# Optimization experiments

Measured on AMD Instinct MI355X. Metric: run time of the kernel, lower is better.

The kernel has to match this reference:

```python
import jax, jax.numpy as jnp
import numpy as np

B, N, D = 4, 128, 128
EPS = 1e-6

def setup_inputs() -> dict:
    key = jax.random.key(0)
    ks = jax.random.split(key, 10)
    q = jax.random.normal(ks[0], (B, N, D), dtype=jnp.float32)
    mu = jax.random.normal(ks[1], (B, N, 3, D), dtype=jnp.float32)
    Wij = jax.random.normal(ks[2], (B, N, N, 3 * D), dtype=jnp.float32)
    dir_ij = jax.random.normal(ks[3], (B, N, N, 3), dtype=jnp.float32)
    mask_ij = jax.random.uniform(ks[4], (B, N, N), dtype=jnp.float32)
    # RMSNorm weight initialized to zeros (torch code: nn.Parameter(torch.zeros(dim)))
    norm_w = jnp.zeros((D,), dtype=jnp.float32)
    # Dense 1 (GLU variant): Linear(D, 2D)
    s1 = 1.0 / np.sqrt(D)
    W1 = jax.random.uniform(ks[5], (2 * D, D), minval=-s1, maxval=s1, dtype=jnp.float32)
    b1 = jax.random.uniform(ks[6], (2 * D,), minval=-s1, maxval=s1, dtype=jnp.float32)
    # Dense 2: Linear(D, 3D), no activation
    W2 = jax.random.uniform(ks[7], (3 * D, D), minval=-s1, maxval=s1, dtype=jnp.float32)
    b2 = jax.random.uniform(ks[8], (3 * D,), minval=-s1, maxval=s1, dtype=jnp.float32)
    return {"q": q, "mu": mu, "Wij": Wij, "dir_ij": dir_ij, "mask_ij": mask_ij,
            "norm_w": norm_w, "W1": W1, "b1": b1, "W2": W2, "b2": b2}

def reference(q, mu, Wij, dir_ij, mask_ij, norm_w, W1, b1, W2, b2):
    # RMSNorm (fp32, unit offset)
    xf = q.astype(jnp.float32)
    var = jnp.mean(xf * xf, axis=-1, keepdims=True)
    h = xf * jax.lax.rsqrt(var + EPS) * (1.0 + norm_w)
    # Dense(D -> D, GLU with silu) then Dense(D -> 3D)
    y = h @ W1.T + b1                      # (B,N,2D)
    a, g = jnp.split(y, 2, axis=-1)
    h2 = jax.nn.silu(a) * jax.nn.sigmoid(g)
    x = h2 @ W2.T + b2                     # (B,N,3D)
    # pairwise broadcast-multiply: xj over neighbor axis j
    x_inter = Wij * x[:, None, :, :] * mask_ij[..., None]   # (B,N,N,3D)
    dq, dmuR, dmumu = jnp.split(x_inter, 3, axis=-1)        # each (B,N,N,D)
    dq = dq.sum(axis=2)                                     # (B,N,D)
    muj = jnp.swapaxes(mu, -1, -2)[:, None]                 # (B,1,N,D,3)
    dmu = (dmuR[..., None] * dir_ij[:, :, :, None, :]
           + dmumu[..., None] * muj).sum(axis=2)            # (B,N,D,3)
    dmu = jnp.swapaxes(dmu, -1, -2)                         # (B,N,3,D)
    return (q + dq, mu + dmu)
```

## Files before the change

kernel.cpp:

```cpp
#include <hip/hip_runtime.h>


#define B_ 4
#define N_ 128
#define D_ 128

typedef __attribute__((ext_vector_type(4))) float float4v;

__device__ __align__(16) float g_x[B_ * N_ * 3 * D_];

__device__ __forceinline__ float sigm(float x) { return 1.0f / (1.0f + __expf(-x)); }

__global__ __launch_bounds__(256) void k1_mlp(
        const float* __restrict__ q, const float* __restrict__ norm_w,
        const float* __restrict__ W1, const float* __restrict__ b1,
        const float* __restrict__ W2, const float* __restrict__ b2) {
    const int row = blockIdx.x;
    const int t   = threadIdx.x;

    __shared__ __align__(16) float hbuf[D_];
    __shared__ __align__(16) float h2buf[D_];
    __shared__ float ybuf[2 * D_];
    __shared__ float red4[4];

    float v  = (t < D_) ? q[(size_t)row * D_ + t] : 0.0f;
    float ss = v * v;
    #pragma unroll
    for (int off = 32; off > 0; off >>= 1) ss += __shfl_down(ss, off);
    if ((t & 63) == 0) red4[t >> 6] = ss;
    __syncthreads();
    float var   = (red4[0] + red4[1] + red4[2] + red4[3]) * (1.0f / D_);
    float scale = rsqrtf(var + 1e-6f);
    if (t < D_) hbuf[t] = v * scale * (1.0f + norm_w[t]);
    __syncthreads();

    float y = b1[t];
    const float4v* wr = (const float4v*)(W1 + (size_t)t * D_);
    #pragma unroll 8
    for (int c = 0; c < D_ / 4; ++c) {
        float4v w4 = wr[c];
        float4v h4 = *(const float4v*)&hbuf[4 * c];
        y += w4.x * h4.x + w4.y * h4.y + w4.z * h4.z + w4.w * h4.w;
    }
    ybuf[t] = y;
    __syncthreads();
    if (t < D_) {
        float a = ybuf[t], g = ybuf[D_ + t];
        h2buf[t] = a * sigm(a) * sigm(g);
    }
    __syncthreads();

    float x0 = b2[t];
    float x1 = (t < D_) ? b2[2 * D_ + t] : 0.0f;
    const float4v* w0 = (const float4v*)(W2 + (size_t)t * D_);
    const float4v* w1 = (const float4v*)(W2 + (size_t)(2 * D_ + (t & (D_ - 1))) * D_);
    #pragma unroll 8
    for (int c = 0; c < D_ / 4; ++c) {
        float4v h4 = *(const float4v*)&h2buf[4 * c];
        float4v a4 = w0[c];
        x0 += a4.x * h4.x + a4.y * h4.y + a4.z * h4.z + a4.w * h4.w;
        if (t < D_) {
            float4v b4 = w1[c];
            x1 += b4.x * h4.x + b4.y * h4.y + b4.z * h4.z + b4.w * h4.w;
        }
    }
    float* xr = g_x + (size_t)row * (3 * D_);
    xr[t] = x0;
    if (t < D_) xr[2 * D_ + t] = x1;
}

__global__ __launch_bounds__(512) void k2_pair(
        const float* __restrict__ q, const float* __restrict__ mu,
        const float* __restrict__ Wij, const float* __restrict__ dir,
        const float* __restrict__ mask, float* __restrict__ out) {
    const int blk  = blockIdx.x;
    const int t    = threadIdx.x;
    const int quad = t & 31;
    const int js   = t >> 5;
    const int b    = blk >> 7;

    const float* Wb  = Wij  + (size_t)blk * (N_ * 3 * D_);
    const float* mb  = mask + (size_t)blk * N_;
    const float* db  = dir  + (size_t)blk * (N_ * 3);
    const float* mub = mu   + (size_t)b * (N_ * 3 * D_);
    const float* xb  = g_x  + (size_t)b * (N_ * 3 * D_);

    float4v aq = {0.f, 0.f, 0.f, 0.f};
    float4v a0 = {0.f, 0.f, 0.f, 0.f};
    float4v a1 = {0.f, 0.f, 0.f, 0.f};
    float4v a2 = {0.f, 0.f, 0.f, 0.f};

    #pragma unroll 2
    for (int it = 0; it < 8; ++it) {
        const int j = it * 16 + js;
        const float m  = mb[j];
        const float e0 = db[3 * j + 0];
        const float e1 = db[3 * j + 1];
        const float e2 = db[3 * j + 2];

        const size_t base = (size_t)j * (3 * D_) + 4 * quad;
        float4v wq = __builtin_nontemporal_load((const float4v*)(Wb + base));
        float4v wR = __builtin_nontemporal_load((const float4v*)(Wb + base + D_));
        float4v wm = __builtin_nontemporal_load((const float4v*)(Wb + base + 2 * D_));
        float4v xq = *(const float4v*)(xb + base);
        float4v xR = *(const float4v*)(xb + base + D_);
        float4v xm = *(const float4v*)(xb + base + 2 * D_);
        float4v u0 = *(const float4v*)(mub + base);
        float4v u1 = *(const float4v*)(mub + base + D_);
        float4v u2 = *(const float4v*)(mub + base + 2 * D_);

        #pragma unroll
        for (int i = 0; i < 4; ++i) {
            aq[i] += wq[i] * (xq[i] * m);
            float tR = wR[i] * (xR[i] * m);
            float tm = wm[i] * (xm[i] * m);
            a0[i] += tR * e0 + tm * u0[i];
            a1[i] += tR * e1 + tm * u1[i];
            a2[i] += tR * e2 + tm * u2[i];
        }
    }

    #pragma unroll
    for (int i = 0; i < 4; ++i) {
        aq[i] += __shfl_down(aq[i], 32);
        a0[i] += __shfl_down(a0[i], 32);
        a1[i] += __shfl_down(a1[i], 32);
        a2[i] += __shfl_down(a2[i], 32);
    }

    __shared__ __align__(16) float ws[8][4][D_];
    const int w = t >> 6, l = t & 63;
    if (l < 32) {
        *(float4v*)&ws[w][0][4 * quad] = aq;
        *(float4v*)&ws[w][1][4 * quad] = a0;
        *(float4v*)&ws[w][2][4 * quad] = a1;
        *(float4v*)&ws[w][3][4 * quad] = a2;
    }
    __syncthreads();

    const int comp = t >> 7;
    const int ch   = t & 127;
    float s = 0.f;
    #pragma unroll
    for (int wv = 0; wv < 8; ++wv) s += ws[wv][comp][ch];

    if (comp == 0) {
        const size_t o = (size_t)blk * D_ + ch;
        __builtin_nontemporal_store(q[o] + s, out + o);
    } else {
        const size_t o = ((size_t)blk * 3 + (comp - 1)) * D_ + ch;
        __builtin_nontemporal_store(mu[o] + s, out + (size_t)(B_ * N_ * D_) + o);
    }
}

extern "C" void kernel_launch(void* const* d_in, const int* in_sizes, int n_in,
                              void* d_out, int out_size, void* d_ws, size_t ws_size,
                              hipStream_t stream) {
    const float* q     = (const float*)d_in[0];
    const float* mu    = (const float*)d_in[1];
    const float* Wij   = (const float*)d_in[2];
    const float* dir   = (const float*)d_in[3];
    const float* mask  = (const float*)d_in[4];
    const float* normw = (const float*)d_in[5];
    const float* W1    = (const float*)d_in[6];
    const float* b1    = (const float*)d_in[7];
    const float* W2    = (const float*)d_in[8];
    const float* b2    = (const float*)d_in[9];

    k1_mlp <<<B_ * N_, 256, 0, stream>>>(q, normw, W1, b1, W2, b2);
    k2_pair<<<B_ * N_, 512, 0, stream>>>(q, mu, Wij, dir, mask, (float*)d_out);
}
```

Before: 195.7 us.

## Split pair kernel across channel halves with register prefetch and staged mask/dir

The pair kernel now launches twice as many 256-thread blocks, each covering half the channels of one (b,i) row. It stages mask and direction values into shared memory and software-pipelines the Wij/x/mu loads one iteration ahead in registers. The reduction switches to xor shuffles plus a smaller shared buffer. The aim is more blocks in flight and more memory-level parallelism for the dominant Wij stream, at the cost of higher register pressure and duplicated x/mu reads across the two halves.

```diff
diff --git a/kernel.cpp b/kernel.cpp
--- a/kernel.cpp
+++ b/kernel.cpp
@@ -69,86 +69,122 @@
     if (t < D_) xr[2 * D_ + t] = x1;
 }
 
-__global__ __launch_bounds__(512) void k2_pair(
+__global__ __launch_bounds__(256, 4) void k2_pair(
         const float* __restrict__ q, const float* __restrict__ mu,
         const float* __restrict__ Wij, const float* __restrict__ dir,
         const float* __restrict__ mask, float* __restrict__ out) {
     const int blk  = blockIdx.x;
+    const int bi   = blk >> 1;
+    const int h    = blk & 1;
+    const int b    = bi >> 7;
     const int t    = threadIdx.x;
-    const int quad = t & 31;
-    const int js   = t >> 5;
-    const int b    = blk >> 7;
-
-    const float* Wb  = Wij  + (size_t)blk * (N_ * 3 * D_);
-    const float* mb  = mask + (size_t)blk * N_;
-    const float* db  = dir  + (size_t)blk * (N_ * 3);
+    const int quad = t & 15;
+    const int js   = t >> 4;
+    const int choff = h * 64 + 4 * quad;
+
+    const float* Wb  = Wij  + (size_t)bi * (N_ * 3 * D_);
     const float* mub = mu   + (size_t)b * (N_ * 3 * D_);
     const float* xb  = g_x  + (size_t)b * (N_ * 3 * D_);
+
+    __shared__ float smsk[N_];
+    __shared__ float sdir[3 * N_];
+    {
+        const float* mb = mask + (size_t)bi * N_;
+        const float* db = dir  + (size_t)bi * (N_ * 3);
+        if (t < N_) smsk[t] = mb[t];
+        for (int idx = t; idx < 3 * N_; idx += 256) sdir[idx] = db[idx];
+    }
+    __syncthreads();
 
     float4v aq = {0.f, 0.f, 0.f, 0.f};
     float4v a0 = {0.f, 0.f, 0.f, 0.f};
     float4v a1 = {0.f, 0.f, 0.f, 0.f};
     float4v a2 = {0.f, 0.f, 0.f, 0.f};
 
-    #pragma unroll 2
+    float4v wqA, wRA, wmA, xqA, xRA, xmA, u0A, u1A, u2A;
+    float4v wqB, wRB, wmB, xqB, xRB, xmB, u0B, u1B, u2B;
+
+    {
+        const size_t base = (size_t)js * (3 * D_) + choff;
+        wqA = __builtin_nontemporal_load((const float4v*)(Wb + base));
+        wRA = __builtin_nontemporal_load((const float4v*)(Wb + base + D_));
+        wmA = __builtin_nontemporal_load((const float4v*)(Wb + base + 2 * D_));
+        xqA = *(const float4v*)(xb + base);
+        xRA = *(const float4v*)(xb + base + D_);
+        xmA = *(const float4v*)(xb + base + 2 * D_);
+        u0A = *(const float4v*)(mub + base);
+        u1A = *(const float4v*)(mub + base + D_);
+        u2A = *(const float4v*)(mub + base + 2 * D_);
+    }
+
+    #pragma unroll
     for (int it = 0; it < 8; ++it) {
+        if (it < 7) {
+            const int jn = (it + 1) * 16 + js;
+            const size_t base = (size_t)jn * (3 * D_) + choff;
+            wqB = __builtin_nontemporal_load((const float4v*)(Wb + base));
+            wRB = __builtin_nontemporal_load((const float4v*)(Wb + base + D_));
+            wmB = __builtin_nontemporal_load((const float4v*)(Wb + base + 2 * D_));
+            xqB = *(const float4v*)(xb + base);
+            xRB = *(const float4v*)(xb + base + D_);
+            xmB = *(const float4v*)(xb + base + 2 * D_);
+            u0B = *(const float4v*)(mub + base);
+            u1B = *(const float4v*)(mub + base + D_);
+            u2B = *(const float4v*)(mub + base + 2 * D_);
+        }
+
         const int j = it * 16 + js;
-        const float m  = mb[j];
-        const float e0 = db[3 * j + 0];
-        const float e1 = db[3 * j + 1];
-        const float e2 = db[3 * j + 2];
-
-        const size_t base = (size_t)j * (3 * D_) + 4 * quad;
-        float4v wq = __builtin_nontemporal_load((const float4v*)(Wb + base));
-        float4v wR = __builtin_nontemporal_load((const float4v*)(Wb + base + D_));
-        float4v wm = __builtin_nontemporal_load((const float4v*)(Wb + base + 2 * D_));
-        float4v xq = *(const float4v*)(xb + base);
-        float4v xR = *(const float4v*)(xb + base + D_);
-        float4v xm = *(const float4v*)(xb + base + 2 * D_);
-        float4v u0 = *(const float4v*)(mub + base);
-        float4v u1 = *(const float4v*)(mub + base + D_);
-        float4v u2 = *(const float4v*)(mub + base + 2 * D_);
+        const float m  = smsk[j];
+        const float e0 = sdir[3 * j + 0];
+        const float e1 = sdir[3 * j + 1];
+        const float e2 = sdir[3 * j + 2];
 
         #pragma unroll
         for (int i = 0; i < 4; ++i) {
-            aq[i] += wq[i] * (xq[i] * m);
-            float tR = wR[i] * (xR[i] * m);
-            float tm = wm[i] * (xm[i] * m);
-            a0[i] += tR * e0 + tm * u0[i];
-            a1[i] += tR * e1 + tm * u1[i];
-            a2[i] += tR * e2 + tm * u2[i];
+            aq[i] += wqA[i] * (xqA[i] * m);
+            float tR = wRA[i] * (xRA[i] * m);
+            float tm = wmA[i] * (xmA[i] * m);
+            a0[i] += tR * e0 + tm * u0A[i];
+            a1[i] += tR * e1 + tm * u1A[i];
+            a2[i] += tR * e2 + tm * u2A[i];
         }
+
+        wqA = wqB; wRA = wRB; wmA = wmB;
+        xqA = xqB; xRA = xRB; xmA = xmB;
+        u0A = u0B; u1A = u1B; u2A = u2B;
     }
 
     #pragma unroll
     for (int i = 0; i < 4; ++i) {
-        aq[i] += __shfl_down(aq[i], 32);
-        a0[i] += __shfl_down(a0[i], 32);
-        a1[i] += __shfl_down(a1[i], 32);
-        a2[i] += __shfl_down(a2[i], 32);
-    }
-
-    __shared__ __align__(16) float ws[8][4][D_];
+        aq[i] += __shfl_xor(aq[i], 16, 64);
+        aq[i] += __shfl_xor(aq[i], 32, 64);
+        a0[i] += __shfl_xor(a0[i], 16, 64);
+        a0[i] += __shfl_xor(a0[i], 32, 64);
+        a1[i] += __shfl_xor(a1[i], 16, 64);
+        a1[i] += __shfl_xor(a1[i], 32, 64);
+        a2[i] += __shfl_xor(a2[i], 16, 64);
+        a2[i] += __shfl_xor(a2[i], 32, 64);
+    }
+
+    __shared__ __align__(16) float ws[4][4][64];
     const int w = t >> 6, l = t & 63;
-    if (l < 32) {
-        *(float4v*)&ws[w][0][4 * quad] = aq;
-        *(float4v*)&ws[w][1][4 * quad] = a0;
-        *(float4v*)&ws[w][2][4 * quad] = a1;
-        *(float4v*)&ws[w][3][4 * quad] = a2;
-    }
-    __syncthreads();
-
-    const int comp = t >> 7;
-    const int ch   = t & 127;
-    float s = 0.f;
-    #pragma unroll
-    for (int wv = 0; wv < 8; ++wv) s += ws[wv][comp][ch];
+    if (l < 16) {
+        *(float4v*)&ws[w][0][4 * l] = aq;
+        *(float4v*)&ws[w][1][4 * l] = a0;
+        *(float4v*)&ws[w][2][4 * l] = a1;
+        *(float4v*)&ws[w][3][4 * l] = a2;
+    }
+    __syncthreads();
+
+    const int comp = t >> 6;
+    const int ch   = t & 63;
+    float s = ws[0][comp][ch] + ws[1][comp][ch] + ws[2][comp][ch] + ws[3][comp][ch];
 
     if (comp == 0) {
-        const size_t o = (size_t)blk * D_ + ch;
+        const size_t o = (size_t)bi * D_ + h * 64 + ch;
         __builtin_nontemporal_store(q[o] + s, out + o);
     } else {
-        const size_t o = ((size_t)blk * 3 + (comp - 1)) * D_ + ch;
+        const size_t o = ((size_t)bi * 3 + (comp - 1)) * D_ + h * 64 + ch;
         __builtin_nontemporal_store(mu[o] + s, out + (size_t)(B_ * N_ * D_) + o);
     }
 }
@@ -167,6 +203,6 @@
     const float* W2    = (const float*)d_in[8];
     const float* b2    = (const float*)d_in[9];
 
-    k1_mlp <<<B_ * N_, 256, 0, stream>>>(q, normw, W1, b1, W2, b2);
-    k2_pair<<<B_ * N_, 512, 0, stream>>>(q, mu, Wij, dir, mask, (float*)d_out);
+    k1_mlp <<<B_ * N_,     256, 0, stream>>>(q, normw, W1, b1, W2, b2);
+    k2_pair<<<B_ * N_ * 2, 256, 0, stream>>>(q, mu, Wij, dir, mask, (float*)d_out);
 }
```

Result: slower. 203.7 us (+4.1%).

## Tile pair kernel over four query rows and channel slices to reuse x/mu

Applied to the files above, without the earlier changes.

Restructures the pairwise kernel so each block handles four i rows and a 32-channel slice, loading x and mu once per j and reusing them across the four rows. Mask and direction values are staged in shared memory, and the j reduction uses xor shuffles plus a small shared reduction. This is meant to cut repeated L2 reads of x and mu. In exchange it uses more registers per thread, fewer threads per block, and shorter contiguous segments per Wij access.

```diff
diff --git a/kernel.cpp b/kernel.cpp
--- a/kernel.cpp
+++ b/kernel.cpp
@@ -4,6 +4,7 @@
 #define B_ 4
 #define N_ 128
 #define D_ 128
+#define I_ 4
 
 typedef __attribute__((ext_vector_type(4))) float float4v;
 
@@ -69,39 +70,54 @@
     if (t < D_) xr[2 * D_ + t] = x1;
 }
 
-__global__ __launch_bounds__(512) void k2_pair(
+__global__ __launch_bounds__(256) void k2_pair(
         const float* __restrict__ q, const float* __restrict__ mu,
         const float* __restrict__ Wij, const float* __restrict__ dir,
         const float* __restrict__ mask, float* __restrict__ out) {
-    const int blk  = blockIdx.x;
-    const int t    = threadIdx.x;
-    const int quad = t & 31;
-    const int js   = t >> 5;
-    const int b    = blk >> 7;
-
-    const float* Wb  = Wij  + (size_t)blk * (N_ * 3 * D_);
-    const float* mb  = mask + (size_t)blk * N_;
-    const float* db  = dir  + (size_t)blk * (N_ * 3);
-    const float* mub = mu   + (size_t)b * (N_ * 3 * D_);
-    const float* xb  = g_x  + (size_t)b * (N_ * 3 * D_);
-
-    float4v aq = {0.f, 0.f, 0.f, 0.f};
-    float4v a0 = {0.f, 0.f, 0.f, 0.f};
-    float4v a1 = {0.f, 0.f, 0.f, 0.f};
-    float4v a2 = {0.f, 0.f, 0.f, 0.f};
-
-    #pragma unroll 2
-    for (int it = 0; it < 8; ++it) {
-        const int j = it * 16 + js;
-        const float m  = mb[j];
-        const float e0 = db[3 * j + 0];
-        const float e1 = db[3 * j + 1];
-        const float e2 = db[3 * j + 2];
-
-        const size_t base = (size_t)j * (3 * D_) + 4 * quad;
-        float4v wq = __builtin_nontemporal_load((const float4v*)(Wb + base));
-        float4v wR = __builtin_nontemporal_load((const float4v*)(Wb + base + D_));
-        float4v wm = __builtin_nontemporal_load((const float4v*)(Wb + base + 2 * D_));
+    const int blk = blockIdx.x;
+    const int cs  = blk & 3;
+    const int ti  = (blk >> 2) & 31;
+    const int b   = blk >> 7;
+    const int i0  = ti * I_;
+    const int t   = threadIdx.x;
+    const int quad = t & 7;
+    const int js   = t >> 3;
+    const int choff = cs * 32 + 4 * quad;
+
+    const float* xb  = g_x + (size_t)b * (N_ * 3 * D_);
+    const float* mub = mu  + (size_t)b * (N_ * 3 * D_);
+
+    const float* Wb0 = Wij + (size_t)((b * N_ + i0 + 0) * N_) * (3 * D_);
+    const float* Wb1 = Wij + (size_t)((b * N_ + i0 + 1) * N_) * (3 * D_);
+    const float* Wb2 = Wij + (size_t)((b * N_ + i0 + 2) * N_) * (3 * D_);
+    const float* Wb3 = Wij + (size_t)((b * N_ + i0 + 3) * N_) * (3 * D_);
+
+    __shared__ float smsk[I_][N_];
+    __shared__ float sdir[I_][3 * N_];
+    for (int idx = t; idx < I_ * N_; idx += 256) {
+        const int ii = idx >> 7, j = idx & (N_ - 1);
+        smsk[ii][j] = mask[(size_t)(b * N_ + i0 + ii) * N_ + j];
+    }
+    for (int idx = t; idx < I_ * 3 * N_; idx += 256) {
+        const int ii = idx / (3 * N_), r = idx % (3 * N_);
+        sdir[ii][r] = dir[(size_t)(b * N_ + i0 + ii) * (3 * N_) + r];
+    }
+    __syncthreads();
+
+    float4v aq[I_], a0[I_], a1[I_], a2[I_];
+    #pragma unroll
+    for (int ii = 0; ii < I_; ++ii) {
+        aq[ii] = {0.f, 0.f, 0.f, 0.f};
+        a0[ii] = {0.f, 0.f, 0.f, 0.f};
+        a1[ii] = {0.f, 0.f, 0.f, 0.f};
+        a2[ii] = {0.f, 0.f, 0.f, 0.f};
+    }
+
+    #pragma unroll
+    for (int jt = 0; jt < 4; ++jt) {
+        const int j = jt * 32 + js;
+        const size_t base = (size_t)j * (3 * D_) + choff;
+
         float4v xq = *(const float4v*)(xb + base);
         float4v xR = *(const float4v*)(xb + base + D_);
         float4v xm = *(const float4v*)(xb + base + 2 * D_);
@@ -110,46 +126,75 @@
         float4v u2 = *(const float4v*)(mub + base + 2 * D_);
 
         #pragma unroll
-        for (int i = 0; i < 4; ++i) {
-            aq[i] += wq[i] * (xq[i] * m);
-            float tR = wR[i] * (xR[i] * m);
-            float tm = wm[i] * (xm[i] * m);
-            a0[i] += tR * e0 + tm * u0[i];
-            a1[i] += tR * e1 + tm * u1[i];
-            a2[i] += tR * e2 + tm * u2[i];
-        }
-    }
-
-    #pragma unroll
-    for (int i = 0; i < 4; ++i) {
-        aq[i] += __shfl_down(aq[i], 32);
-        a0[i] += __shfl_down(a0[i], 32);
-        a1[i] += __shfl_down(a1[i], 32);
-        a2[i] += __shfl_down(a2[i], 32);
-    }
-
-    __shared__ __align__(16) float ws[8][4][D_];
+        for (int ii = 0; ii < I_; ++ii) {
+            const float* Wb = (ii == 0) ? Wb0 : (ii == 1) ? Wb1 : (ii == 2) ? Wb2 : Wb3;
+            float4v wq = __builtin_nontemporal_load((const float4v*)(Wb + base));
+            float4v wR = __builtin_nontemporal_load((const float4v*)(Wb + base + D_));
+            float4v wm = __builtin_nontemporal_load((const float4v*)(Wb + base + 2 * D_));
+            const float m  = smsk[ii][j];
+            const float e0 = sdir[ii][3 * j + 0];
+            const float e1 = sdir[ii][3 * j + 1];
+            const float e2 = sdir[ii][3 * j + 2];
+            #pragma unroll
+            for (int c = 0; c < 4; ++c) {
+                aq[ii][c] += wq[c] * (xq[c] * m);
+                float tR = wR[c] * (xR[c] * m);
+                float tm = wm[c] * (xm[c] * m);
+                a0[ii][c] += tR * e0 + tm * u0[c];
+                a1[ii][c] += tR * e1 + tm * u1[c];
+                a2[ii][c] += tR * e2 + tm * u2[c];
+            }
+        }
+    }
+
+    #pragma unroll
+    for (int ii = 0; ii < I_; ++ii) {
+        #pragma unroll
+        for (int c = 0; c < 4; ++c) {
+            aq[ii][c] += __shfl_xor(aq[ii][c], 8, 64);
+            aq[ii][c] += __shfl_xor(aq[ii][c], 16, 64);
+            aq[ii][c] += __shfl_xor(aq[ii][c], 32, 64);
+            a0[ii][c] += __shfl_xor(a0[ii][c], 8, 64);
+            a0[ii][c] += __shfl_xor(a0[ii][c], 16, 64);
+            a0[ii][c] += __shfl_xor(a0[ii][c], 32, 64);
+            a1[ii][c] += __shfl_xor(a1[ii][c], 8, 64);
+            a1[ii][c] += __shfl_xor(a1[ii][c], 16, 64);
+            a1[ii][c] += __shfl_xor(a1[ii][c], 32, 64);
+            a2[ii][c] += __shfl_xor(a2[ii][c], 8, 64);
+            a2[ii][c] += __shfl_xor(a2[ii][c], 16, 64);
+            a2[ii][c] += __shfl_xor(a2[ii][c], 32, 64);
+        }
+    }
+
+    __shared__ __align__(16) float red[4][I_][4][32];
     const int w = t >> 6, l = t & 63;
-    if (l < 32) {
-        *(float4v*)&ws[w][0][4 * quad] = aq;
-        *(float4v*)&ws[w][1][4 * quad] = a0;
-        *(float4v*)&ws[w][2][4 * quad] = a1;
-        *(float4v*)&ws[w][3][4 * quad] = a2;
-    }
-    __syncthreads();
-
-    const int comp = t >> 7;
-    const int ch   = t & 127;
-    float s = 0.f;
-    #pragma unroll
-    for (int wv = 0; wv < 8; ++wv) s += ws[wv][comp][ch];
-
-    if (comp == 0) {
-        const size_t o = (size_t)blk * D_ + ch;
-        __builtin_nontemporal_store(q[o] + s, out + o);
-    } else {
-        const size_t o = ((size_t)blk * 3 + (comp - 1)) * D_ + ch;
-        __builtin_nontemporal_store(mu[o] + s, out + (size_t)(B_ * N_ * D_) + o);
+    if (l < 8) {
+        #pragma unroll
+        for (int ii = 0; ii < I_; ++ii) {
+            *(float4v*)&red[w][ii][0][4 * l] = aq[ii];
+            *(float4v*)&red[w][ii][1][4 * l] = a0[ii];
+            *(float4v*)&red[w][ii][2][4 * l] = a1[ii];
+            *(float4v*)&red[w][ii][3][4 * l] = a2[ii];
+        }
+    }
+    __syncthreads();
+
+    #pragma unroll
+    for (int rep = 0; rep < 2; ++rep) {
+        const int idx  = t + rep * 256;
+        const int comp = idx >> 7;
+        const int ii   = (idx >> 5) & 3;
+        const int ch   = idx & 31;
+        const float s = red[0][ii][comp][ch] + red[1][ii][comp][ch]
+                      + red[2][ii][comp][ch] + red[3][ii][comp][ch];
+        const int gi = b * N_ + i0 + ii;
+        if (comp == 0) {
+            const size_t o = (size_t)gi * D_ + cs * 32 + ch;
+            __builtin_nontemporal_store(q[o] + s, out + o);
+        } else {
+            const size_t o = ((size_t)gi * 3 + (comp - 1)) * D_ + cs * 32 + ch;
+            __builtin_nontemporal_store(mu[o] + s, out + (size_t)(B_ * N_ * D_) + o);
+        }
     }
 }
 
@@ -167,6 +212,7 @@
     const float* W2    = (const float*)d_in[8];
     const float* b2    = (const float*)d_in[9];
 
-    k1_mlp <<<B_ * N_, 256, 0, stream>>>(q, normw, W1, b1, W2, b2);
-    k2_pair<<<B_ * N_, 512, 0, stream>>>(q, mu, Wij, dir, mask, (float*)d_out);
+    k1_mlp <<<B_ * N_,             256, 0, stream>>>(q, normw, W1, b1, W2, b2);
+    k2_pair<<<B_ * (N_ / I_) * 4,  256, 0, stream>>>(q, mu, Wij, dir, mask,
+                                                     (float*)d_out);
 }
```

Result: slower. 201.6 us (+3.1%).
